# Performance work log

Hardware: AMD Instinct MI355X
Metric: run time of the kernel (lower is better)

The kernel has to match this reference:

```python
import jax, jax.numpy as jnp
import numpy as np

EPS = 1e-12
BETA = 3.0
N_TH = 21


def setup_inputs() -> dict:
    key = jax.random.key(0)
    k1, k2 = jax.random.split(key)
    N, C = 65536, 1000
    logits = jax.random.normal(k1, (N, C), dtype=jnp.float32)
    labels = jax.random.randint(k2, (N,), 0, C, dtype=jnp.int64)
    idx = jnp.arange(N, dtype=jnp.int64)
    return {"logits": logits, "labels": labels, "idx": idx, "type": 0}


def _forward(logits, labels):
    # probs / confidences / predictions
    probs = jax.nn.softmax(logits, axis=1)                      # [N, C]
    conf = jnp.max(probs, axis=1)                               # [N]
    preds = jnp.argmax(probs, axis=1)                           # [N]
    # predictive uncertainty (type == 0): entropy of softmax
    unc = -jnp.sum(probs * jnp.log(probs + EPS), axis=-1)       # [N]
    umin, umax = jnp.min(unc), jnp.max(unc)
    th = jnp.linspace(0.0, 1.0, N_TH, dtype=logits.dtype)       # [21]
    unc_th = umin + th * (umax - umin)                          # [21]

    acc = (labels == preds)                                     # [N] bool
    t_unc = jnp.tanh(unc)                                       # [N]
    certain = unc[None, :] <= unc_th[:, None]                   # [21, N]
    a = acc[None, :]

    zero = jnp.zeros((), logits.dtype)
    n_ac = jnp.sum(jnp.where(a & certain, conf * (1.0 - t_unc), zero), axis=1)
    n_au = jnp.sum(jnp.where(a & ~certain, conf * t_unc, zero), axis=1)
    n_ic = jnp.sum(jnp.where(~a & certain, (1.0 - conf) * (1.0 - t_unc), zero), axis=1)
    n_iu = jnp.sum(jnp.where(~a & ~certain, (1.0 - conf) * t_unc, zero), axis=1)

    avu = (n_ac + n_iu) / (n_ac + n_au + n_ic + n_iu + EPS)     # [21]
    # sklearn.metrics.auc == trapezoidal rule over (th, avu)
    auc_avu = 0.5 * jnp.sum((avu[1:] + avu[:-1]) * (th[1:] - th[:-1]))
    # original wraps auc in a fresh tensor -> no grad through the AvU branch
    avu_loss = -BETA * jnp.log(jax.lax.stop_gradient(auc_avu) + EPS)

    logp = jax.nn.log_softmax(logits, axis=1)                   # [N, C]
    ce = -jnp.mean(jnp.take_along_axis(logp, labels[:, None], axis=1))
    return (avu_loss + ce)[None]                                # [1], matches torch


def reference(logits, labels, idx, type) -> jnp.ndarray:
    del idx, type  # idx unused; type=0 path (predictive uncertainty)
    return _forward(logits, labels)
```

## Files before the change

kernel.cpp:

```cpp
#include <hip/hip_runtime.h>
#include <math.h>

#define NROWS 65536
#define NC    1000
#define NTH   21
#define NBLK1 2048

__device__ __forceinline__ void amax2(float va, int ia, float vb, int ib,
                                      float& vo, int& io) {
    bool t = (va >= vb);
    vo = t ? va : vb;
    io = t ? ia : ib;
}

__device__ __forceinline__ void row_process(
        float4 r0, float4 r1, float4 r2, float4 r3,
        int lane, int label, int row,
        float* __restrict__ unc_o, float* __restrict__ confs_o,
        float& mn, float& mx, float& ssum)
{
    int b0 = lane << 2, b1 = (lane + 64) << 2, b2 = (lane + 128) << 2, b3 = (lane + 192) << 2;
    float mA, mB, mC, mD, mt0, mt1, m; int iA, iB, iC, iD, it0, it1, mi;
    {
        float p, q; int pi, qi;
        amax2(r0.x, b0+0, r0.y, b0+1, p, pi); amax2(r0.z, b0+2, r0.w, b0+3, q, qi);
        amax2(p, pi, q, qi, mA, iA);
        amax2(r1.x, b1+0, r1.y, b1+1, p, pi); amax2(r1.z, b1+2, r1.w, b1+3, q, qi);
        amax2(p, pi, q, qi, mB, iB);
        amax2(r2.x, b2+0, r2.y, b2+1, p, pi); amax2(r2.z, b2+2, r2.w, b2+3, q, qi);
        amax2(p, pi, q, qi, mC, iC);
        amax2(r3.x, b3+0, r3.y, b3+1, p, pi); amax2(r3.z, b3+2, r3.w, b3+3, q, qi);
        amax2(p, pi, q, qi, mD, iD);
    }
    amax2(mA, iA, mB, iB, mt0, it0);
    amax2(mC, iC, mD, iD, mt1, it1);
    amax2(mt0, it0, mt1, it1, m, mi);

    #pragma unroll
    for (int off = 1; off < 64; off <<= 1) {
        float om = __shfl_xor(m, off, 64);
        int   oi = __shfl_xor(mi, off, 64);
        if (om > m || (om == m && oi < mi)) { m = om; mi = oi; }
    }

    float se = 0.f, sx = 0.f;
#define ACCUM(v) { float t_ = (v) - m; float e_ = __expf(t_); se += e_; sx = fmaf(e_, t_, sx); }
    ACCUM(r0.x) ACCUM(r0.y) ACCUM(r0.z) ACCUM(r0.w)
    ACCUM(r1.x) ACCUM(r1.y) ACCUM(r1.z) ACCUM(r1.w)
    ACCUM(r2.x) ACCUM(r2.y) ACCUM(r2.z) ACCUM(r2.w)
    ACCUM(r3.x) ACCUM(r3.y) ACCUM(r3.z) ACCUM(r3.w)
#undef ACCUM
    #pragma unroll
    for (int off = 1; off < 64; off <<= 1) {
        se += __shfl_xor(se, off, 64);
        sx += __shfl_xor(sx, off, 64);
    }

    float Z    = se;
    float logZ = logf(Z);
    float conf = 1.0f / Z;
    float uncv = logZ - sx / Z;

    int f4 = label >> 2, slot = label & 3, it = f4 >> 6;
    float4 q = (it == 0) ? r0 : (it == 1) ? r1 : (it == 2) ? r2 : r3;
    float cand = (slot == 0) ? q.x : (slot == 1) ? q.y : (slot == 2) ? q.z : q.w;
    float xl = __shfl(cand, f4 & 63, 64);
    float lp = (xl - m) - logZ;

    if (lane == 0) {
        unc_o[row]   = uncv;
        confs_o[row] = (mi == label) ? conf : -conf;
    }
    mn = fminf(mn, uncv);
    mx = fmaxf(mx, uncv);
    ssum += lp;
}

#define LOADROW(P, q0, q1, q2, q3) \
    q0 = (P)[lane]; q1 = (P)[lane + 64]; q2 = (P)[lane + 128]; \
    q3 = make_float4(-1e30f, -1e30f, -1e30f, -1e30f); \
    if (lane < 58) q3 = (P)[lane + 192];

__global__ __launch_bounds__(256, 4) void k1_rowstats(
        const float* __restrict__ logits, const int* __restrict__ labels,
        float* __restrict__ unc_o, float* __restrict__ confs_o,
        float* __restrict__ blk_mn, float* __restrict__ blk_mx, float* __restrict__ blk_s,
        float* __restrict__ bins)
{
    if (blockIdx.x == 0 && threadIdx.x < 88) bins[threadIdx.x] = 0.f;

    const int wave = threadIdx.x >> 6;
    const int lane = threadIdx.x & 63;
    const int row0 = (blockIdx.x * 4 + wave) * 8;
    const float4* p = (const float4*)(logits + (size_t)row0 * NC);

    int lab0 = labels[row0],     lab1 = labels[row0 + 1];
    int lab2 = labels[row0 + 2], lab3 = labels[row0 + 3];
    int lab4 = labels[row0 + 4], lab5 = labels[row0 + 5];
    int lab6 = labels[row0 + 6], lab7 = labels[row0 + 7];

    float mn = 1e30f, mx = -1e30f, ssum = 0.f;
    float4 a0, a1, a2, a3, b0, b1, b2, b3;

    LOADROW(p,         a0, a1, a2, a3)
    LOADROW(p + 250,   b0, b1, b2, b3)
    row_process(a0, a1, a2, a3, lane, lab0, row0,     unc_o, confs_o, mn, mx, ssum);
    LOADROW(p + 500,   a0, a1, a2, a3)
    row_process(b0, b1, b2, b3, lane, lab1, row0 + 1, unc_o, confs_o, mn, mx, ssum);
    LOADROW(p + 750,   b0, b1, b2, b3)
    row_process(a0, a1, a2, a3, lane, lab2, row0 + 2, unc_o, confs_o, mn, mx, ssum);
    LOADROW(p + 1000,  a0, a1, a2, a3)
    row_process(b0, b1, b2, b3, lane, lab3, row0 + 3, unc_o, confs_o, mn, mx, ssum);
    LOADROW(p + 1250,  b0, b1, b2, b3)
    row_process(a0, a1, a2, a3, lane, lab4, row0 + 4, unc_o, confs_o, mn, mx, ssum);
    LOADROW(p + 1500,  a0, a1, a2, a3)
    row_process(b0, b1, b2, b3, lane, lab5, row0 + 5, unc_o, confs_o, mn, mx, ssum);
    LOADROW(p + 1750,  b0, b1, b2, b3)
    row_process(a0, a1, a2, a3, lane, lab6, row0 + 6, unc_o, confs_o, mn, mx, ssum);
    row_process(b0, b1, b2, b3, lane, lab7, row0 + 7, unc_o, confs_o, mn, mx, ssum);

    __shared__ float s_mn[4], s_mx[4], s_s[4];
    if (lane == 0) { s_mn[wave] = mn; s_mx[wave] = mx; s_s[wave] = ssum; }
    __syncthreads();
    if (threadIdx.x == 0) {
        blk_mn[blockIdx.x] = fminf(fminf(s_mn[0], s_mn[1]), fminf(s_mn[2], s_mn[3]));
        blk_mx[blockIdx.x] = fmaxf(fmaxf(s_mx[0], s_mx[1]), fmaxf(s_mx[2], s_mx[3]));
        blk_s [blockIdx.x] = (s_s[0] + s_s[1]) + (s_s[2] + s_s[3]);
    }
}

__global__ __launch_bounds__(256) void k23_hist(
        const float* __restrict__ blk_mn, const float* __restrict__ blk_mx,
        const float* __restrict__ blk_s,
        const float* __restrict__ unc, const float* __restrict__ confs,
        float* __restrict__ ce_sum, float* __restrict__ bins)
{
    __shared__ float h[88];
    __shared__ float smn[4], smx[4], ss[4];
    for (int i = threadIdx.x; i < 88; i += 256) h[i] = 0.f;

    float mn = 1e30f, mx = -1e30f, s = 0.f;
    for (int i = threadIdx.x; i < NBLK1; i += 256) {
        mn = fminf(mn, blk_mn[i]);
        mx = fmaxf(mx, blk_mx[i]);
        s += blk_s[i];
    }
    #pragma unroll
    for (int off = 1; off < 64; off <<= 1) {
        mn = fminf(mn, __shfl_xor(mn, off, 64));
        mx = fmaxf(mx, __shfl_xor(mx, off, 64));
        s += __shfl_xor(s, off, 64);
    }
    int wave = threadIdx.x >> 6;
    if ((threadIdx.x & 63) == 0) { smn[wave] = mn; smx[wave] = mx; ss[wave] = s; }
    __syncthreads();
    if (threadIdx.x == 0) {
        mn = fminf(fminf(smn[0], smn[1]), fminf(smn[2], smn[3]));
        mx = fmaxf(fmaxf(smx[0], smx[1]), fmaxf(smx[2], smx[3]));
        smn[0] = mn; smx[0] = mx;
        if (blockIdx.x == 0) {
            *ce_sum = (ss[0] + ss[1]) + (ss[2] + ss[3]);
        }
    }
    __syncthreads();
    float umin = smn[0];
    float umax = smx[0];
    float du = umax - umin;

    int i = blockIdx.x * 256 + threadIdx.x;
    float u  = unc[i];
    float cs = confs[i];
    float conf = fabsf(cs);
    bool  acc  = cs > 0.f;
    float tu = tanhf(u);

    int b = NTH;
    #pragma unroll
    for (int t = NTH - 1; t >= 0; --t) {
        float th = umin + ((float)t * 0.05f) * du;
        if (u <= th) b = t;
    }
    float w = acc ? conf : (1.f - conf);
    int base = acc ? 0 : 44;
    atomicAdd(&h[base + b],       w * (1.f - tu));
    atomicAdd(&h[base + 22 + b],  w * tu);
    __syncthreads();
    for (int i2 = threadIdx.x; i2 < 88; i2 += 256) {
        float v = h[i2];
        if (v != 0.f) atomicAdd(&bins[i2], v);
    }
}

__global__ void k4_final(const float* __restrict__ bins, const float* __restrict__ ce_sum,
                         float* __restrict__ out)
{
    if (threadIdx.x != 0 || blockIdx.x != 0) return;
    float tot_au = 0.f, tot_iu = 0.f;
    for (int b = 0; b < 22; ++b) { tot_au += bins[22 + b]; tot_iu += bins[66 + b]; }
    float cac = 0.f, cau = 0.f, cic = 0.f, ciu = 0.f;
    float avu[NTH];
    for (int t = 0; t < NTH; ++t) {
        cac += bins[t]; cau += bins[22 + t]; cic += bins[44 + t]; ciu += bins[66 + t];
        float nac = cac, nau = tot_au - cau, nic = cic, niu = tot_iu - ciu;
        avu[t] = (nac + niu) / (nac + nau + nic + niu + 1e-12f);
    }
    float auc = 0.f;
    for (int t = 0; t + 1 < NTH; ++t) auc += 0.5f * (avu[t + 1] + avu[t]) * 0.05f;
    float avu_loss = -3.0f * logf(auc + 1e-12f);
    float ce = -(*ce_sum) / (float)NROWS;
    out[0] = avu_loss + ce;
}

extern "C" void kernel_launch(void* const* d_in, const int* in_sizes, int n_in,
                              void* d_out, int out_size, void* d_ws, size_t ws_size,
                              hipStream_t stream)
{
    const float* logits = (const float*)d_in[0];
    const int*   labels = (const int*)d_in[1];
    float* ws    = (float*)d_ws;
    float* unc   = ws;
    float* confs = ws + NROWS;
    float* bins  = ws + 2 * NROWS;
    float* ce_sum = ws + 2 * NROWS + 1024;
    float* blk_mn = ws + 2 * NROWS + 4096;
    float* blk_mx = blk_mn + NBLK1;
    float* blk_s  = blk_mx + NBLK1;

    hipLaunchKernelGGL(k1_rowstats, dim3(NBLK1), dim3(256), 0, stream,
                       logits, labels, unc, confs, blk_mn, blk_mx, blk_s, bins);
    hipLaunchKernelGGL(k23_hist, dim3(NROWS / 256), dim3(256), 0, stream,
                       blk_mn, blk_mx, blk_s, unc, confs, ce_sum, bins);
    hipLaunchKernelGGL(k4_final, dim3(1), dim3(64), 0, stream,
                       bins, ce_sum, (float*)d_out);
}
```

Baseline: 377.4 us.

## Fuse final reduction via ticket, simplify argmax, use nontemporal loads

The final scalar kernel is folded into the histogram kernel. A global ticket counter lets the last block to finish compute the AvU/AUC loss, which removes one launch. The row argmax becomes a plain fmax reduction followed by an index search for the first matching element, and the logits are read with nontemporal loads. Exp accumulation is split into independent partial sums and log uses the fast intrinsic. This costs a threadfence and an atomic ticket per block, and slightly changes floating-point rounding.

```diff
diff --git a/kernel.cpp b/kernel.cpp
--- a/kernel.cpp
+++ b/kernel.cpp
@@ -6,11 +6,10 @@
 #define NTH   21
 #define NBLK1 2048
 
-__device__ __forceinline__ void amax2(float va, int ia, float vb, int ib,
-                                      float& vo, int& io) {
-    bool t = (va >= vb);
-    vo = t ? va : vb;
-    io = t ? ia : ib;
+typedef float f32x4_t __attribute__((ext_vector_type(4)));
+__device__ __forceinline__ float4 ntload4(const float4* p) {
+    f32x4_t v = __builtin_nontemporal_load((const f32x4_t*)p);
+    return make_float4(v.x, v.y, v.z, v.w);
 }
 
 __device__ __forceinline__ void row_process(
@@ -19,37 +18,39 @@
         float* __restrict__ unc_o, float* __restrict__ confs_o,
         float& mn, float& mx, float& ssum)
 {
+    float mA = fmaxf(fmaxf(r0.x, r0.y), fmaxf(r0.z, r0.w));
+    float mB = fmaxf(fmaxf(r1.x, r1.y), fmaxf(r1.z, r1.w));
+    float mC = fmaxf(fmaxf(r2.x, r2.y), fmaxf(r2.z, r2.w));
+    float mD = fmaxf(fmaxf(r3.x, r3.y), fmaxf(r3.z, r3.w));
+    float m  = fmaxf(fmaxf(mA, mB), fmaxf(mC, mD));
+    #pragma unroll
+    for (int off = 1; off < 64; off <<= 1)
+        m = fmaxf(m, __shfl_xor(m, off, 64));
+
     int b0 = lane << 2, b1 = (lane + 64) << 2, b2 = (lane + 128) << 2, b3 = (lane + 192) << 2;
-    float mA, mB, mC, mD, mt0, mt1, m; int iA, iB, iC, iD, it0, it1, mi;
-    {
-        float p, q; int pi, qi;
-        amax2(r0.x, b0+0, r0.y, b0+1, p, pi); amax2(r0.z, b0+2, r0.w, b0+3, q, qi);
-        amax2(p, pi, q, qi, mA, iA);
-        amax2(r1.x, b1+0, r1.y, b1+1, p, pi); amax2(r1.z, b1+2, r1.w, b1+3, q, qi);
-        amax2(p, pi, q, qi, mB, iB);
-        amax2(r2.x, b2+0, r2.y, b2+1, p, pi); amax2(r2.z, b2+2, r2.w, b2+3, q, qi);
-        amax2(p, pi, q, qi, mC, iC);
-        amax2(r3.x, b3+0, r3.y, b3+1, p, pi); amax2(r3.z, b3+2, r3.w, b3+3, q, qi);
-        amax2(p, pi, q, qi, mD, iD);
-    }
-    amax2(mA, iA, mB, iB, mt0, it0);
-    amax2(mC, iC, mD, iD, mt1, it1);
-    amax2(mt0, it0, mt1, it1, m, mi);
-
-    #pragma unroll
-    for (int off = 1; off < 64; off <<= 1) {
-        float om = __shfl_xor(m, off, 64);
-        int   oi = __shfl_xor(mi, off, 64);
-        if (om > m || (om == m && oi < mi)) { m = om; mi = oi; }
-    }
-
-    float se = 0.f, sx = 0.f;
-#define ACCUM(v) { float t_ = (v) - m; float e_ = __expf(t_); se += e_; sx = fmaf(e_, t_, sx); }
-    ACCUM(r0.x) ACCUM(r0.y) ACCUM(r0.z) ACCUM(r0.w)
-    ACCUM(r1.x) ACCUM(r1.y) ACCUM(r1.z) ACCUM(r1.w)
-    ACCUM(r2.x) ACCUM(r2.y) ACCUM(r2.z) ACCUM(r2.w)
-    ACCUM(r3.x) ACCUM(r3.y) ACCUM(r3.z) ACCUM(r3.w)
-#undef ACCUM
+    int mi = 0x7fffffff;
+    if (r3.w == m) mi = b3 + 3;  if (r3.z == m) mi = b3 + 2;
+    if (r3.y == m) mi = b3 + 1;  if (r3.x == m) mi = b3 + 0;
+    if (r2.w == m) mi = b2 + 3;  if (r2.z == m) mi = b2 + 2;
+    if (r2.y == m) mi = b2 + 1;  if (r2.x == m) mi = b2 + 0;
+    if (r1.w == m) mi = b1 + 3;  if (r1.z == m) mi = b1 + 2;
+    if (r1.y == m) mi = b1 + 1;  if (r1.x == m) mi = b1 + 0;
+    if (r0.w == m) mi = b0 + 3;  if (r0.z == m) mi = b0 + 2;
+    if (r0.y == m) mi = b0 + 1;  if (r0.x == m) mi = b0 + 0;
+    #pragma unroll
+    for (int off = 1; off < 64; off <<= 1)
+        mi = min(mi, __shfl_xor(mi, off, 64));
+
+#define ACC4(r, se, sx) { \
+    float ta = r.x - m, tb = r.y - m, tc = r.z - m, td = r.w - m; \
+    float ea = __expf(ta), eb = __expf(tb), ec = __expf(tc), ed = __expf(td); \
+    se = (ea + eb) + (ec + ed); \
+    sx = fmaf(ea, ta, fmaf(eb, tb, fmaf(ec, tc, ed * td))); }
+    float seA, sxA, seB, sxB, seC, sxC, seD, sxD;
+    ACC4(r0, seA, sxA) ACC4(r1, seB, sxB) ACC4(r2, seC, sxC) ACC4(r3, seD, sxD)
+#undef ACC4
+    float se = (seA + seB) + (seC + seD);
+    float sx = (sxA + sxB) + (sxC + sxD);
     #pragma unroll
     for (int off = 1; off < 64; off <<= 1) {
         se += __shfl_xor(se, off, 64);
@@ -57,9 +58,10 @@
     }
 
     float Z    = se;
-    float logZ = logf(Z);
-    float conf = 1.0f / Z;
-    float uncv = logZ - sx / Z;
+    float logZ = __logf(Z);
+    float rZ   = 1.0f / Z;
+    float conf = rZ;
+    float uncv = fmaf(-sx, rZ, logZ);
 
     int f4 = label >> 2, slot = label & 3, it = f4 >> 6;
     float4 q = (it == 0) ? r0 : (it == 1) ? r1 : (it == 2) ? r2 : r3;
@@ -77,17 +79,20 @@
 }
 
 #define LOADROW(P, q0, q1, q2, q3) \
-    q0 = (P)[lane]; q1 = (P)[lane + 64]; q2 = (P)[lane + 128]; \
+    q0 = ntload4((P) + lane); q1 = ntload4((P) + lane + 64); q2 = ntload4((P) + lane + 128); \
     q3 = make_float4(-1e30f, -1e30f, -1e30f, -1e30f); \
-    if (lane < 58) q3 = (P)[lane + 192];
+    if (lane < 58) q3 = ntload4((P) + lane + 192);
 
 __global__ __launch_bounds__(256, 4) void k1_rowstats(
         const float* __restrict__ logits, const int* __restrict__ labels,
         float* __restrict__ unc_o, float* __restrict__ confs_o,
         float* __restrict__ blk_mn, float* __restrict__ blk_mx, float* __restrict__ blk_s,
-        float* __restrict__ bins)
-{
-    if (blockIdx.x == 0 && threadIdx.x < 88) bins[threadIdx.x] = 0.f;
+        float* __restrict__ bins, unsigned* __restrict__ ticket)
+{
+    if (blockIdx.x == 0) {
+        if (threadIdx.x < 88) bins[threadIdx.x] = 0.f;
+        if (threadIdx.x == 88) *ticket = 0u;
+    }
 
     const int wave = threadIdx.x >> 6;
     const int lane = threadIdx.x & 63;
@@ -133,7 +138,8 @@
         const float* __restrict__ blk_mn, const float* __restrict__ blk_mx,
         const float* __restrict__ blk_s,
         const float* __restrict__ unc, const float* __restrict__ confs,
-        float* __restrict__ ce_sum, float* __restrict__ bins)
+        float* __restrict__ bins, unsigned* __restrict__ ticket,
+        float* __restrict__ out)
 {
     __shared__ float h[88];
     __shared__ float smn[4], smx[4], ss[4];
@@ -155,12 +161,9 @@
     if ((threadIdx.x & 63) == 0) { smn[wave] = mn; smx[wave] = mx; ss[wave] = s; }
     __syncthreads();
     if (threadIdx.x == 0) {
-        mn = fminf(fminf(smn[0], smn[1]), fminf(smn[2], smn[3]));
-        mx = fmaxf(fmaxf(smx[0], smx[1]), fmaxf(smx[2], smx[3]));
-        smn[0] = mn; smx[0] = mx;
-        if (blockIdx.x == 0) {
-            *ce_sum = (ss[0] + ss[1]) + (ss[2] + ss[3]);
-        }
+        smn[0] = fminf(fminf(smn[0], smn[1]), fminf(smn[2], smn[3]));
+        smx[0] = fmaxf(fmaxf(smx[0], smx[1]), fmaxf(smx[2], smx[3]));
+        ss[0]  = (ss[0] + ss[1]) + (ss[2] + ss[3]);
     }
     __syncthreads();
     float umin = smn[0];
@@ -189,26 +192,31 @@
         float v = h[i2];
         if (v != 0.f) atomicAdd(&bins[i2], v);
     }
-}
-
-__global__ void k4_final(const float* __restrict__ bins, const float* __restrict__ ce_sum,
-                         float* __restrict__ out)
-{
-    if (threadIdx.x != 0 || blockIdx.x != 0) return;
-    float tot_au = 0.f, tot_iu = 0.f;
-    for (int b = 0; b < 22; ++b) { tot_au += bins[22 + b]; tot_iu += bins[66 + b]; }
-    float cac = 0.f, cau = 0.f, cic = 0.f, ciu = 0.f;
-    float avu[NTH];
-    for (int t = 0; t < NTH; ++t) {
-        cac += bins[t]; cau += bins[22 + t]; cic += bins[44 + t]; ciu += bins[66 + t];
-        float nac = cac, nau = tot_au - cau, nic = cic, niu = tot_iu - ciu;
-        avu[t] = (nac + niu) / (nac + nau + nic + niu + 1e-12f);
-    }
-    float auc = 0.f;
-    for (int t = 0; t + 1 < NTH; ++t) auc += 0.5f * (avu[t + 1] + avu[t]) * 0.05f;
-    float avu_loss = -3.0f * logf(auc + 1e-12f);
-    float ce = -(*ce_sum) / (float)NROWS;
-    out[0] = avu_loss + ce;
+
+    __threadfence();
+    __syncthreads();
+    if (threadIdx.x == 0) {
+        unsigned t = atomicAdd(ticket, 1u);
+        if (t == (unsigned)(gridDim.x - 1)) {
+            __threadfence();
+            float tot_au = 0.f, tot_iu = 0.f;
+            for (int bq = 0; bq < 22; ++bq) { tot_au += bins[22 + bq]; tot_iu += bins[66 + bq]; }
+            float cac = 0.f, cau = 0.f, cic = 0.f, ciu = 0.f;
+            float avu[NTH];
+            #pragma unroll
+            for (int tt = 0; tt < NTH; ++tt) {
+                cac += bins[tt]; cau += bins[22 + tt]; cic += bins[44 + tt]; ciu += bins[66 + tt];
+                float nac = cac, nau = tot_au - cau, nic = cic, niu = tot_iu - ciu;
+                avu[tt] = (nac + niu) / (nac + nau + nic + niu + 1e-12f);
+            }
+            float auc = 0.f;
+            #pragma unroll
+            for (int tt = 0; tt + 1 < NTH; ++tt) auc += 0.5f * (avu[tt + 1] + avu[tt]) * 0.05f;
+            float avu_loss = -3.0f * logf(auc + 1e-12f);
+            float ce = -ss[0] / (float)NROWS;
+            out[0] = avu_loss + ce;
+        }
+    }
 }
 
 extern "C" void kernel_launch(void* const* d_in, const int* in_sizes, int n_in,
@@ -221,15 +229,13 @@
     float* unc   = ws;
     float* confs = ws + NROWS;
     float* bins  = ws + 2 * NROWS;
-    float* ce_sum = ws + 2 * NROWS + 1024;
+    unsigned* ticket = (unsigned*)(ws + 2 * NROWS + 96);
     float* blk_mn = ws + 2 * NROWS + 4096;
     float* blk_mx = blk_mn + NBLK1;
     float* blk_s  = blk_mx + NBLK1;
 
     hipLaunchKernelGGL(k1_rowstats, dim3(NBLK1), dim3(256), 0, stream,
-                       logits, labels, unc, confs, blk_mn, blk_mx, blk_s, bins);
+                       logits, labels, unc, confs, blk_mn, blk_mx, blk_s, bins, ticket);
     hipLaunchKernelGGL(k23_hist, dim3(NROWS / 256), dim3(256), 0, stream,
-                       blk_mn, blk_mx, blk_s, unc, confs, ce_sum, bins);
-    hipLaunchKernelGGL(k4_final, dim3(1), dim3(64), 0, stream,
-                       bins, ce_sum, (float*)d_out);
-}
+                       blk_mn, blk_mx, blk_s, unc, confs, bins, ticket, (float*)d_out);
+}
```

Result: faster. 358.6 us (-5.0%).
